# Optimization experiments

Hardware: AMD Instinct MI355X
Metric: run time of the kernel (lower is better)

Reference implementation:

```python
import jax, jax.numpy as jnp
import numpy as np

B, L_IMG, L_TXT, DM, H, D = 1, 4096, 512, 3072, 24, 128
EPS = 1e-6


def _rms(x, scale):
    # flax nnx RMSNorm: x * rsqrt(mean(x^2) + eps) * scale
    var = jnp.mean(jnp.square(x), axis=-1, keepdims=True)
    return x * jax.lax.rsqrt(var + EPS) * scale


def _qkv(x, W, qn, kn):
    b, l = x.shape[:2]
    qkv = (x @ W).reshape(b, l, 3, H, D).transpose(2, 0, 3, 1, 4)  # [3,B,H,L,D]
    q, k, v = qkv[0], qkv[1], qkv[2]
    return _rms(q, qn), _rms(k, kn), v


def setup_inputs() -> dict:
    key = jax.random.key(0)
    ks = jax.random.split(key, 8)
    s = 0.02
    return {
        "hidden_states": jax.random.normal(ks[0], (B, L_IMG, DM), jnp.float32),
        "encoder_hidden_states": jax.random.normal(ks[1], (B, L_TXT, DM), jnp.float32),
        "image_rotary_emb": jax.random.normal(ks[2], (L_TXT + L_IMG, D // 2, 4), jnp.float32),
        "W_iqkv": jax.random.normal(ks[3], (DM, 3 * H * D), jnp.float32) * s,
        "W_eqkv": jax.random.normal(ks[4], (DM, 3 * H * D), jnp.float32) * s,
        "W_iproj": jax.random.normal(ks[5], (H * D, DM), jnp.float32) * s,
        "b_iproj": jnp.zeros((DM,), jnp.float32),
        "W_eproj": jax.random.normal(ks[6], (H * D, DM), jnp.float32) * s,
        "b_eproj": jnp.zeros((DM,), jnp.float32),
        "qn_scale": jnp.ones((D,), jnp.float32),
        "kn_scale": jnp.ones((D,), jnp.float32),
        "eqn_scale": jnp.ones((D,), jnp.float32),
        "ekn_scale": jnp.ones((D,), jnp.float32),
    }


def reference(hidden_states, encoder_hidden_states, image_rotary_emb,
              W_iqkv, W_eqkv, W_iproj, b_iproj, W_eproj, b_eproj,
              qn_scale, kn_scale, eqn_scale, ekn_scale):
    scale = D ** -0.5
    l_txt = encoder_hidden_states.shape[1]

    q, k, v = _qkv(hidden_states, W_iqkv, qn_scale, kn_scale)           # [B,H,L_img,D]
    eq, ek, ev = _qkv(encoder_hidden_states, W_eqkv, eqn_scale, ekn_scale)

    q = jnp.concatenate((eq, q), axis=2)   # [B,H,L,D], L = L_txt + L_img
    k = jnp.concatenate((ek, k), axis=2)
    v = jnp.concatenate((ev, v), axis=2)

    # RoPE: freqs_cis [L, D/2, 2, 2]
    fc = image_rotary_emb.reshape(image_rotary_emb.shape[0], image_rotary_emb.shape[1], 2, 2)

    def rope(x):
        x_ = x.reshape(*x.shape[:-1], -1, 1, 2)  # [B,H,L,D/2,1,2]
        out = fc[..., 0] * x_[..., 0] + fc[..., 1] * x_[..., 1]  # [B,H,L,D/2,2]
        return out.reshape(*x.shape).astype(x.dtype)

    q, k = rope(q), rope(k)

    # flatten heads into feature dim BEFORE attention (faithful to original)
    def merge(x):
        b, h, l, d = x.shape
        return x.transpose(0, 2, 1, 3).reshape(b, l, h * d)

    qm, km, vm = merge(q), merge(k), merge(v)  # [B,L,H*D]

    attn = jax.nn.softmax(jnp.einsum('bqd,bkd->bqk', qm, km) * scale, axis=-1)
    out = jnp.einsum('bqk,bkd->bqd', attn, vm)  # [B,L,H*D]

    ctx_out, img_out = out[:, :l_txt], out[:, l_txt:]
    img_out = img_out @ W_iproj + b_iproj
    ctx_out = ctx_out @ W_eproj + b_eproj
    return img_out, ctx_out
```

## Files before the change

### kernel.cpp

```cpp
#include <hip/hip_runtime.h>
#include <hip/hip_bf16.h>
#include <cstdint>

typedef __attribute__((ext_vector_type(8))) short u16x8;
typedef _Float16 f16_t;
typedef __attribute__((ext_vector_type(8))) f16_t f16x8;
typedef __attribute__((ext_vector_type(4))) float f32x4;

#define L_TOT 4608
#define L_TXT 512
#define L_IMG 4096
#define NH 24
#define HD 128
#define DMODEL 3072
#define NQKV 9216
#define LOG2E 1.44269504088896340736f
#define S_SHIFT 32.0f

__device__ __forceinline__ ushort f2h(float f) {
  union { f16_t h; ushort u; } c; c.h = (f16_t)f; return c.u;
}
__device__ __forceinline__ float h2f(ushort u) {
  union { ushort u; f16_t h; } c; c.u = u; return (float)c.h;
}
__device__ __forceinline__ void gload16(const ushort* g, ushort* l) {
  __builtin_amdgcn_global_load_lds((const __attribute__((address_space(1))) void*)g,
                                   (__attribute__((address_space(3))) void*)l, 16, 0, 0);
}

__global__ void cvt_f32_f16(const float* __restrict__ src, ushort* __restrict__ dst,
                            int n8) {
  const int i = blockIdx.x * 256 + threadIdx.x;
  if (i >= n8) return;
  const f32x4 a = *(const f32x4*)(src + (size_t)i * 8);
  const f32x4 b = *(const f32x4*)(src + (size_t)i * 8 + 4);
  alignas(16) ushort o[8];
#pragma unroll
  for (int j = 0; j < 4; ++j) { o[j] = f2h(a[j]); o[4 + j] = f2h(b[j]); }
  *(u16x8*)(dst + (size_t)i * 8) = *(const u16x8*)o;
}

__global__ void tconv_w(const float* __restrict__ src, int C, int c0,
                        ushort* __restrict__ dst) {
  __shared__ ushort tile[64][72];
  const int nb = blockIdx.x << 6, kb = blockIdx.y << 6;
  const int t = threadIdx.x;
  const int lr = t >> 2, lc = (t & 3) << 4;
  const float* sp = src + (size_t)(kb + lr) * C + c0 + nb + lc;
  const f32x4 v0 = *(const f32x4*)sp;
  const f32x4 v1 = *(const f32x4*)(sp + 4);
  const f32x4 v2 = *(const f32x4*)(sp + 8);
  const f32x4 v3 = *(const f32x4*)(sp + 12);
#pragma unroll
  for (int i = 0; i < 4; ++i) {
    tile[lr][lc + i]      = f2h(v0[i]);
    tile[lr][lc + 4 + i]  = f2h(v1[i]);
    tile[lr][lc + 8 + i]  = f2h(v2[i]);
    tile[lr][lc + 12 + i] = f2h(v3[i]);
  }
  __syncthreads();
  const int cl = t & 63, rb = (t >> 6) << 4;
  alignas(16) ushort o[16];
#pragma unroll
  for (int i = 0; i < 16; ++i) o[i] = tile[rb + i][cl];
  ushort* dp = dst + (size_t)(nb + cl) * DMODEL + kb + rb;
  *(u16x8*)dp       = *(const u16x8*)o;
  *(u16x8*)(dp + 8) = *(const u16x8*)(o + 8);
}

__global__ void tconv_h(const ushort* __restrict__ src, ushort* __restrict__ dst,
                        int R, int C) {
  __shared__ ushort tile[64][72];
  const int r0 = blockIdx.y << 6, c0 = blockIdx.x << 6;
  const int t = threadIdx.x;
  const int lr = t >> 2, lc = (t & 3) << 4;
  const ushort* sp = src + (size_t)(r0 + lr) * C + c0 + lc;
  const u16x8 v0 = *(const u16x8*)sp;
  const u16x8 v1 = *(const u16x8*)(sp + 8);
#pragma unroll
  for (int i = 0; i < 8; ++i) {
    tile[lr][lc + i]     = ((const ushort*)&v0)[i];
    tile[lr][lc + 8 + i] = ((const ushort*)&v1)[i];
  }
  __syncthreads();
  const int cl = t & 63, rb = (t >> 6) << 4;
  alignas(16) ushort o[16];
#pragma unroll
  for (int i = 0; i < 16; ++i) o[i] = tile[rb + i][cl];
  ushort* dp = dst + (size_t)(c0 + cl) * R + r0 + rb;
  *(u16x8*)dp       = *(const u16x8*)o;
  *(u16x8*)(dp + 8) = *(const u16x8*)(o + 8);
}

template <int MODE>
__global__ __launch_bounds__(512, 2) void gemm256(
    const ushort* __restrict__ A, int lda,
    const ushort* __restrict__ BtLo, const ushort* __restrict__ BtHi, int ldb,
    int N, int K, void* __restrict__ out0, ushort* __restrict__ out1,
    ushort* __restrict__ out2, const float* __restrict__ biasLo,
    const float* __restrict__ biasHi, int n_base) {
  __shared__ __align__(16) ushort lds[2][2][2][8192];
  int lin = blockIdx.y * gridDim.x + blockIdx.x;
  {
    const int nwg = gridDim.x * gridDim.y;
    const int q8 = nwg >> 3, r8 = nwg & 7;
    const int xcd = lin & 7, idx = lin >> 3;
    lin = (xcd < r8 ? xcd * (q8 + 1) : r8 * (q8 + 1) + (xcd - r8) * q8) + idx;
  }
  const int m0 = (lin % gridDim.x) << 8, n0 = (lin / gridDim.x) << 8;
  const ushort* Bt = (m0 < L_TXT) ? BtLo : BtHi;
  const int tid = threadIdx.x, w = tid >> 6, lane = tid & 63;
  const int wm = w >> 2, wn = w & 3;
  const int lr = lane & 15, g4 = lane >> 4;
  const int srow = lane >> 2;
  const int soff = 8 * ((lane & 3) ^ ((lane >> 3) & 3));
  f32x4 acc[8][4];
#pragma unroll
  for (int a = 0; a < 8; ++a)
#pragma unroll
    for (int b = 0; b < 4; ++b) acc[a][b] = (f32x4){0.f, 0.f, 0.f, 0.f};
  const int nt = K >> 6;

  auto stageA = [&](int h, int kt, int b) {
#pragma unroll
    for (int i = 0; i < 2; ++i) {
      const int j = w * 2 + i;
      gload16(A + (size_t)(m0 + 16 * j + srow) * lda + (kt << 6) + 32 * h + soff,
              &lds[b][h][0][j * 512]);
    }
  };
  auto stageB = [&](int h, int kt, int b) {
#pragma unroll
    for (int i = 0; i < 2; ++i) {
      const int j = w * 2 + i;
      gload16(Bt + (size_t)(n0 + 16 * j + srow) * ldb + (kt << 6) + 32 * h + soff,
              &lds[b][h][1][j * 512]);
    }
  };
  auto readA = [&](int h, int mi, int b) -> f16x8 {
    const int row = wm * 128 + mi * 16 + lr;
    const int byte = row * 64 + ((g4 ^ ((row >> 1) & 3)) << 4);
    return *(const f16x8*)((const char*)&lds[b][h][0][0] + byte);
  };
  auto readB = [&](int h, int ni, int b) -> f16x8 {
    const int row = wn * 64 + ni * 16 + lr;
    const int byte = row * 64 + ((g4 ^ ((row >> 1) & 3)) << 4);
    return *(const f16x8*)((const char*)&lds[b][h][1][0] + byte);
  };

  stageA(0, 0, 0); stageB(0, 0, 0); stageA(1, 0, 0); stageB(1, 0, 0);

  for (int kt = 0; kt < nt; ++kt) {
    const int c = kt & 1, sb = c ^ 1;
    const int st = (kt + 1 < nt) ? kt + 1 : 0;
    f16x8 bf[4], af[8];
    asm volatile("s_waitcnt vmcnt(4)" ::: "memory");
    asm volatile("s_barrier" ::: "memory");
    stageA(0, st, sb); stageB(0, st, sb);
#pragma unroll
    for (int ni = 0; ni < 4; ++ni) bf[ni] = readB(0, ni, c);
#pragma unroll
    for (int m = 0; m < 8; ++m) af[m] = readA(0, m, c);
    __builtin_amdgcn_s_setprio(1);
#pragma unroll
    for (int m = 0; m < 8; ++m)
#pragma unroll
      for (int ni = 0; ni < 4; ++ni)
        acc[m][ni] = __builtin_amdgcn_mfma_f32_16x16x32_f16(af[m], bf[ni], acc[m][ni], 0, 0, 0);
    __builtin_amdgcn_s_setprio(0);
    asm volatile("s_waitcnt vmcnt(4)" ::: "memory");
    asm volatile("s_barrier" ::: "memory");
    stageA(1, st, sb); stageB(1, st, sb);
#pragma unroll
    for (int ni = 0; ni < 4; ++ni) bf[ni] = readB(1, ni, c);
#pragma unroll
    for (int m = 0; m < 8; ++m) af[m] = readA(1, m, c);
    __builtin_amdgcn_s_setprio(1);
#pragma unroll
    for (int m = 0; m < 8; ++m)
#pragma unroll
      for (int ni = 0; ni < 4; ++ni)
        acc[m][ni] = __builtin_amdgcn_mfma_f32_16x16x32_f16(af[m], bf[ni], acc[m][ni], 0, 0, 0);
    __builtin_amdgcn_s_setprio(0);
  }

  const int rb = (lane >> 4) << 2;
  const int cl = lane & 15;
  if (MODE == 0) {
    const int g = n_base + n0;
    const int which = g / DMODEL;
    const int col0 = g - which * DMODEL;
    ushort* dst = (which == 0) ? (ushort*)out0 : (which == 1) ? out1 : out2;
#pragma unroll
    for (int mi = 0; mi < 8; ++mi)
#pragma unroll
      for (int j = 0; j < 4; ++j) {
        const int l = m0 + wm * 128 + mi * 16 + rb + j;
        const size_t rbase = (size_t)l * DMODEL + col0 + wn * 64 + cl;
#pragma unroll
        for (int ni = 0; ni < 4; ++ni) dst[rbase + ni * 16] = f2h(acc[mi][ni][j]);
      }
  } else if (MODE == 1) {
    float* outf = (float*)out0;
    const float* bias = (m0 < L_TXT) ? biasLo : biasHi;
    const int rofs = (m0 < L_TXT) ? L_IMG : -L_TXT;
    float bv[4];
#pragma unroll
    for (int ni = 0; ni < 4; ++ni) bv[ni] = bias[n0 + wn * 64 + ni * 16 + cl];
#pragma unroll
    for (int mi = 0; mi < 8; ++mi)
#pragma unroll
      for (int j = 0; j < 4; ++j) {
        const int r = m0 + wm * 128 + mi * 16 + rb + j + rofs;
        const size_t rbase = (size_t)r * N + n0 + wn * 64 + cl;
#pragma unroll
        for (int ni = 0; ni < 4; ++ni) outf[rbase + ni * 16] = acc[mi][ni][j] + bv[ni];
      }
  } else {
    ushort* outb = (ushort*)out0;
    const float sh = (MODE == 3) ? S_SHIFT : 0.0f;
#pragma unroll
    for (int mi = 0; mi < 8; ++mi)
#pragma unroll
      for (int j = 0; j < 4; ++j) {
        const int r = m0 + wm * 128 + mi * 16 + rb + j;
        const size_t rbase = (size_t)r * N + n0 + wn * 64 + cl;
#pragma unroll
        for (int ni = 0; ni < 4; ++ni) outb[rbase + ni * 16] = f2h(acc[mi][ni][j] - sh);
      }
  }
}

__global__ void norm_rope(ushort* __restrict__ Q, ushort* __restrict__ Kg,
                          const float* __restrict__ rope,
                          const float* __restrict__ qn, const float* __restrict__ kn,
                          const float* __restrict__ eqn, const float* __restrict__ ekn) {
  const int idx = (blockIdx.x << 2) + (threadIdx.x >> 6);
  const int lane = threadIdx.x & 63;
  const int h = idx % NH, l = idx / NH;
  const float* qsc = (l < L_TXT) ? eqn : qn;
  const float* ksc = (l < L_TXT) ? ekn : kn;
  const size_t base = (size_t)l * DMODEL + h * HD + (lane << 1);
  const f32x4 fcv = *(const f32x4*)(rope + ((size_t)l * 64 + lane) * 4);
  const float fa = fcv[0], fb = fcv[1], fc = fcv[2], fd = fcv[3];
  const float s0 = qsc[lane << 1], s1 = qsc[(lane << 1) + 1];
  const float t0 = ksc[lane << 1], t1 = ksc[(lane << 1) + 1];
  {
    const uint32_t qv = *(const uint32_t*)&Q[base];
    float x0 = h2f((ushort)(qv & 0xffff)), x1 = h2f((ushort)(qv >> 16));
    float ss = x0 * x0 + x1 * x1;
#pragma unroll
    for (int m = 1; m < 64; m <<= 1) ss += __shfl_xor(ss, m);
    const float r = rsqrtf(ss * (1.0f / 128.0f) + 1e-6f);
    x0 *= r * s0;
    x1 *= r * s1;
    const float o0 = (fa * x0 + fb * x1) * 0.08838834764831845f;
    const float o1 = (fc * x0 + fd * x1) * 0.08838834764831845f;
    *(uint32_t*)&Q[base] = (uint32_t)f2h(o0) | ((uint32_t)f2h(o1) << 16);
  }
  {
    const uint32_t kv = *(const uint32_t*)&Kg[base];
    float x0 = h2f((ushort)(kv & 0xffff)), x1 = h2f((ushort)(kv >> 16));
    float ss = x0 * x0 + x1 * x1;
#pragma unroll
    for (int m = 1; m < 64; m <<= 1) ss += __shfl_xor(ss, m);
    const float r = rsqrtf(ss * (1.0f / 128.0f) + 1e-6f);
    x0 *= r * t0;
    x1 *= r * t1;
    const float o0 = fa * x0 + fb * x1;
    const float o1 = fc * x0 + fd * x1;
    *(uint32_t*)&Kg[base] = (uint32_t)f2h(o0) | ((uint32_t)f2h(o1) << 16);
  }
}

__global__ void softmax_rows(ushort* __restrict__ S) {
  const int r = blockIdx.x, tid = threadIdx.x;
  ushort* Sr = S + (size_t)r * L_TOT;
  float v[18];
  float m = -3.0e38f;
#pragma unroll
  for (int j = 0; j < 18; ++j) { v[j] = h2f(Sr[tid + (j << 8)]); m = fmaxf(m, v[j]); }
#pragma unroll
  for (int o = 1; o < 64; o <<= 1) m = fmaxf(m, __shfl_xor(m, o));
  __shared__ float redm[4], reds[4];
  const int wave = tid >> 6, lane = tid & 63;
  if (lane == 0) redm[wave] = m;
  __syncthreads();
  m = fmaxf(fmaxf(redm[0], redm[1]), fmaxf(redm[2], redm[3]));
  float s = 0.f;
#pragma unroll
  for (int j = 0; j < 18; ++j) { v[j] = exp2f((v[j] - m) * LOG2E); s += v[j]; }
#pragma unroll
  for (int o = 1; o < 64; o <<= 1) s += __shfl_xor(s, o);
  if (lane == 0) reds[wave] = s;
  __syncthreads();
  const float inv = 1.0f / (reds[0] + reds[1] + reds[2] + reds[3]);
#pragma unroll
  for (int j = 0; j < 18; ++j) Sr[tid + (j << 8)] = f2h(v[j] * inv);
}

extern "C" void kernel_launch(void* const* d_in, const int* in_sizes, int n_in,
                              void* d_out, int out_size, void* d_ws, size_t ws_size,
                              hipStream_t stream) {
  (void)in_sizes; (void)n_in; (void)out_size; (void)ws_size;
  const float* hidden  = (const float*)d_in[0];
  const float* enc     = (const float*)d_in[1];
  const float* rope    = (const float*)d_in[2];
  const float* W_iqkv  = (const float*)d_in[3];
  const float* W_eqkv  = (const float*)d_in[4];
  const float* W_iproj = (const float*)d_in[5];
  const float* b_iproj = (const float*)d_in[6];
  const float* W_eproj = (const float*)d_in[7];
  const float* b_eproj = (const float*)d_in[8];
  const float* qn  = (const float*)d_in[9];
  const float* kn  = (const float*)d_in[10];
  const float* eqn = (const float*)d_in[11];
  const float* ekn = (const float*)d_in[12];
  float* out = (float*)d_out;

  const size_t SZ_S  = (size_t)L_TOT * L_TOT;
  const size_t SZ_LD = (size_t)L_TOT * DMODEL;
  const size_t SZ_WH = (size_t)L_TOT * DMODEL;
  ushort* R0  = (ushort*)d_ws;
  ushort* CF  = R0;
  ushort* S   = R0;
  ushort* QR  = R0 + SZ_S;
  ushort* KR  = QR + SZ_LD;
  ushort* VR  = KR + SZ_LD;
  ushort* VT  = KR;
  ushort* AO  = QR;
  ushort* WTe = (ushort*)out;
  ushort* WTi = WTe + SZ_WH;
  ushort* WPi = R0;
  ushort* WPe = R0 + (size_t)DMODEL * DMODEL;

  dim3 blk(256);
  cvt_f32_f16<<<dim3(L_TXT * DMODEL / 8 / 256), blk, 0, stream>>>(enc, CF,
                                                                  L_TXT * DMODEL / 8);
  cvt_f32_f16<<<dim3(L_IMG * DMODEL / 8 / 256), blk, 0, stream>>>(
      hidden, CF + (size_t)L_TXT * DMODEL, L_IMG * DMODEL / 8);
  for (int h = 0; h < 2; ++h) {
    const int c0 = h * 4608;
    tconv_w<<<dim3(72, 48), blk, 0, stream>>>(W_eqkv, NQKV, c0, WTe);
    tconv_w<<<dim3(72, 48), blk, 0, stream>>>(W_iqkv, NQKV, c0, WTi);
    gemm256<0><<<dim3(L_TOT / 256, 18), dim3(512), 0, stream>>>(
        CF, DMODEL, WTe, WTi, DMODEL, 4608, DMODEL,
        QR, KR, VR, nullptr, nullptr, c0);
  }
  norm_rope<<<dim3(L_TOT * NH / 4), blk, 0, stream>>>(QR, KR, rope, qn, kn, eqn, ekn);
  gemm256<3><<<dim3(L_TOT / 256, L_TOT / 256), dim3(512), 0, stream>>>(
      QR, DMODEL, KR, KR, DMODEL, L_TOT, DMODEL, S, nullptr, nullptr,
      nullptr, nullptr, 0);
  softmax_rows<<<dim3(L_TOT), blk, 0, stream>>>(S);
  tconv_h<<<dim3(48, 72), blk, 0, stream>>>(VR, VT, L_TOT, DMODEL);
  gemm256<2><<<dim3(L_TOT / 256, DMODEL / 256), dim3(512), 0, stream>>>(
      S, L_TOT, VT, VT, L_TOT, DMODEL, L_TOT, AO, nullptr, nullptr,
      nullptr, nullptr, 0);
  tconv_w<<<dim3(48, 48), blk, 0, stream>>>(W_iproj, DMODEL, 0, WPi);
  tconv_w<<<dim3(48, 48), blk, 0, stream>>>(W_eproj, DMODEL, 0, WPe);
  gemm256<1><<<dim3(L_TOT / 256, DMODEL / 256), dim3(512), 0, stream>>>(
      AO, DMODEL, WPe, WPi, DMODEL, DMODEL, DMODEL,
      out, nullptr, nullptr, b_eproj, b_iproj, 0);
}
```

Baseline: 877.1 us.

## Shrink GEMM K-tile to 32 with double-buffered LDS and single-phase loop

The 256x256 GEMM main loop now steps K by 32 instead of 64, using a two-buffer LDS layout of 64 KB instead of 128 KB. Each iteration issues the next tile's global-to-LDS loads first, waits on vmcnt, barriers, runs one batch of MFMAs, then barriers again. The smaller LDS footprint could allow more resident workgroups or lower LDS pressure. The cost is twice as many iterations, barriers and waitcnts per K, with less compute per barrier to hide load latency.

```diff
diff --git a/kernel.cpp b/kernel.cpp
--- a/kernel.cpp
+++ b/kernel.cpp
@@ -99,7 +99,7 @@
     int N, int K, void* __restrict__ out0, ushort* __restrict__ out1,
     ushort* __restrict__ out2, const float* __restrict__ biasLo,
     const float* __restrict__ biasHi, int n_base) {
-  __shared__ __align__(16) ushort lds[2][2][2][8192];
+  __shared__ __align__(16) ushort lds[2][2][8192];
   int lin = blockIdx.y * gridDim.x + blockIdx.x;
   {
     const int nwg = gridDim.x * gridDim.y;
@@ -119,48 +119,48 @@
   for (int a = 0; a < 8; ++a)
 #pragma unroll
     for (int b = 0; b < 4; ++b) acc[a][b] = (f32x4){0.f, 0.f, 0.f, 0.f};
-  const int nt = K >> 6;
-
-  auto stageA = [&](int h, int kt, int b) {
+  const int nt = K >> 5;
+
+  auto stageA = [&](int kt, int b) {
 #pragma unroll
     for (int i = 0; i < 2; ++i) {
       const int j = w * 2 + i;
-      gload16(A + (size_t)(m0 + 16 * j + srow) * lda + (kt << 6) + 32 * h + soff,
-              &lds[b][h][0][j * 512]);
+      gload16(A + (size_t)(m0 + 16 * j + srow) * lda + (kt << 5) + soff,
+              &lds[b][0][j * 512]);
     }
   };
-  auto stageB = [&](int h, int kt, int b) {
+  auto stageB = [&](int kt, int b) {
 #pragma unroll
     for (int i = 0; i < 2; ++i) {
       const int j = w * 2 + i;
-      gload16(Bt + (size_t)(n0 + 16 * j + srow) * ldb + (kt << 6) + 32 * h + soff,
-              &lds[b][h][1][j * 512]);
+      gload16(Bt + (size_t)(n0 + 16 * j + srow) * ldb + (kt << 5) + soff,
+              &lds[b][1][j * 512]);
     }
   };
-  auto readA = [&](int h, int mi, int b) -> f16x8 {
+  auto readA = [&](int mi, int b) -> f16x8 {
     const int row = wm * 128 + mi * 16 + lr;
     const int byte = row * 64 + ((g4 ^ ((row >> 1) & 3)) << 4);
-    return *(const f16x8*)((const char*)&lds[b][h][0][0] + byte);
+    return *(const f16x8*)((const char*)&lds[b][0][0] + byte);
   };
-  auto readB = [&](int h, int ni, int b) -> f16x8 {
+  auto readB = [&](int ni, int b) -> f16x8 {
     const int row = wn * 64 + ni * 16 + lr;
     const int byte = row * 64 + ((g4 ^ ((row >> 1) & 3)) << 4);
-    return *(const f16x8*)((const char*)&lds[b][h][1][0] + byte);
+    return *(const f16x8*)((const char*)&lds[b][1][0] + byte);
   };
 
-  stageA(0, 0, 0); stageB(0, 0, 0); stageA(1, 0, 0); stageB(1, 0, 0);
+  stageA(0, 0); stageB(0, 0);
 
   for (int kt = 0; kt < nt; ++kt) {
     const int c = kt & 1, sb = c ^ 1;
     const int st = (kt + 1 < nt) ? kt + 1 : 0;
-    f16x8 bf[4], af[8];
+    stageA(st, sb); stageB(st, sb);
     asm volatile("s_waitcnt vmcnt(4)" ::: "memory");
     asm volatile("s_barrier" ::: "memory");
-    stageA(0, st, sb); stageB(0, st, sb);
-#pragma unroll
-    for (int ni = 0; ni < 4; ++ni) bf[ni] = readB(0, ni, c);
-#pragma unroll
-    for (int m = 0; m < 8; ++m) af[m] = readA(0, m, c);
+    f16x8 bf[4], af[8];
+#pragma unroll
+    for (int ni = 0; ni < 4; ++ni) bf[ni] = readB(ni, c);
+#pragma unroll
+    for (int m = 0; m < 8; ++m) af[m] = readA(m, c);
     __builtin_amdgcn_s_setprio(1);
 #pragma unroll
     for (int m = 0; m < 8; ++m)
@@ -168,20 +168,7 @@
       for (int ni = 0; ni < 4; ++ni)
         acc[m][ni] = __builtin_amdgcn_mfma_f32_16x16x32_f16(af[m], bf[ni], acc[m][ni], 0, 0, 0);
     __builtin_amdgcn_s_setprio(0);
-    asm volatile("s_waitcnt vmcnt(4)" ::: "memory");
     asm volatile("s_barrier" ::: "memory");
-    stageA(1, st, sb); stageB(1, st, sb);
-#pragma unroll
-    for (int ni = 0; ni < 4; ++ni) bf[ni] = readB(1, ni, c);
-#pragma unroll
-    for (int m = 0; m < 8; ++m) af[m] = readA(1, m, c);
-    __builtin_amdgcn_s_setprio(1);
-#pragma unroll
-    for (int m = 0; m < 8; ++m)
-#pragma unroll
-      for (int ni = 0; ni < 4; ++ni)
-        acc[m][ni] = __builtin_amdgcn_mfma_f32_16x16x32_f16(af[m], bf[ni], acc[m][ni], 0, 0, 0);
-    __builtin_amdgcn_s_setprio(0);
   }
 
   const int rb = (lane >> 4) << 2;
```

Result: slower. 943.9 us (+7.6%).
